# Performance work log

Measured on AMD Instinct MI355X. Metric: run time of the kernel, lower is better.

The kernel has to match this reference:

```python
import jax, jax.numpy as jnp
import numpy as np

EPS = 1e-5
MIN_NORM = 1e-15


def artanh(x):
    return jnp.arctanh(jnp.clip(x, -1.0 + EPS, 1.0 - EPS))


def expmap0(u, c):
    # Poincare ball exponential map at the origin (HGCN style)
    sqrt_c = jnp.sqrt(c)
    u_norm = jnp.maximum(jnp.linalg.norm(u, axis=-1, keepdims=True), MIN_NORM)
    return jnp.tanh(sqrt_c * u_norm) * u / (sqrt_c * u_norm)


def mobius_add(x, y, c):
    x2 = jnp.sum(x * x, axis=-1, keepdims=True)
    y2 = jnp.sum(y * y, axis=-1, keepdims=True)
    xy = jnp.sum(x * y, axis=-1, keepdims=True)
    num = (1.0 + 2.0 * c * xy + c * y2) * x + (1.0 - c * x2) * y
    den = 1.0 + 2.0 * c * xy + (c ** 2) * x2 * y2
    return num / jnp.maximum(den, MIN_NORM)


def sqdist(x, y, c):
    sqrt_c = jnp.sqrt(c)
    ma = mobius_add(-x, y, c)
    dist = (2.0 / sqrt_c) * artanh(sqrt_c * jnp.linalg.norm(ma, axis=-1))
    return dist ** 2


def setup_inputs() -> dict:
    key = jax.random.key(0)
    k1, k2 = jax.random.split(key)
    B, T, N, C, K = 8, 12, 325, 32, 100
    # scale down so points land well inside the unit ball (curvature c=1)
    node_repr = 0.05 * jax.random.normal(k1, (B, T, N, C), dtype=jnp.float32)
    centroid_weight = 0.05 * jax.random.normal(k2, (K, C), dtype=jnp.float32)
    c = jnp.ones((1,), dtype=jnp.float32)
    return {"node_repr": node_repr, "centroid_weight": centroid_weight, "c": c}


def reference(node_repr, centroid_weight, c):
    cc = c[0]
    B, T, N, C = node_repr.shape
    # centroid embedding lookup of arange(K) == the weight table itself
    centroids = expmap0(centroid_weight, cc)          # [K, C]
    x = node_repr[..., None, :]                        # [B, T, N, 1, C]
    node_centroid_dist = sqdist(x, centroids, cc)      # [B, T, N, K] via broadcast
    graph_centroid_dist = jnp.sum(node_centroid_dist, axis=1) / N  # [B, N, K] (faithful to dim=1 in source)
    return graph_centroid_dist, node_centroid_dist
```

## Files before the change

kernel.cpp:

```cpp
#include <hip/hip_runtime.h>

namespace {
constexpr int B = 8, T = 12, N = 325, C = 32, K = 100;
constexpr int NPB = 5;
constexpr int NPAIRS = N / NPB;
constexpr int KT = 7;
constexpr int KP = KT * 16;
constexpr float EPSF = 1e-5f;
constexpr float MIN_NORM = 1e-15f;
}

typedef __attribute__((ext_vector_type(8))) short bf16x8;
typedef __attribute__((ext_vector_type(4))) float f32x4;

__device__ __forceinline__ unsigned short bf16_rne(float x) {
  unsigned int u = __float_as_uint(x);
  unsigned int r = u + 0x7FFFu + ((u >> 16) & 1u);
  return (unsigned short)(r >> 16);
}
__device__ __forceinline__ float bf16_f(unsigned short h) {
  return __uint_as_float(((unsigned int)h) << 16);
}

__global__ __launch_bounds__(320) void hcd_kernel(
    const float* __restrict__ x_g,
    const float* __restrict__ cw,
    const float* __restrict__ cptr,
    float* __restrict__ out0,
    float* __restrict__ out1)
{
  __shared__ unsigned short yh[KP][C];
  __shared__ unsigned short ylo[KP][C];
  __shared__ float y2l[KP];
  __shared__ float x2l[NPB][T];

  const int tid = threadIdx.x;
  const int b  = blockIdx.x / NPAIRS;
  const int np = blockIdx.x % NPAIRS;
  const int n0 = np * NPB;
  const float c  = cptr[0];
  const float sc = sqrtf(c);
  const float inv_c4 = 4.f / c;
  const float HLN2 = 0.34657359028f;
  const float TLOG2E = 2.88539008178f;

  if (tid < KP) {
    float y[C];
    float y2 = 0.f;
    if (tid < K) {
      float u2 = 0.f;
      #pragma unroll
      for (int q = 0; q < C / 4; ++q) {
        float4 v = *(const float4*)(cw + tid * C + 4 * q);
        y[4*q+0] = v.x; y[4*q+1] = v.y; y[4*q+2] = v.z; y[4*q+3] = v.w;
      }
      #pragma unroll
      for (int i = 0; i < C; ++i) u2 = fmaf(y[i], y[i], u2);
      float z = sc * fmaxf(sqrtf(u2), MIN_NORM);
      float E  = exp2f(z * TLOG2E);
      float th = (E - 1.f) * __builtin_amdgcn_rcpf(E + 1.f);
      float f  = th * __builtin_amdgcn_rcpf(z);
      #pragma unroll
      for (int i = 0; i < C; ++i) y[i] *= f;
      y2 = f * f * u2;
    } else {
      #pragma unroll
      for (int i = 0; i < C; ++i) y[i] = 0.f;
    }
    #pragma unroll
    for (int i = 0; i < C; ++i) {
      unsigned short h = bf16_rne(y[i]);
      yh[tid][i]  = h;
      ylo[tid][i] = bf16_rne(y[i] - bf16_f(h));
    }
    y2l[tid] = y2;
  }

  if (tid >= 128 && tid < 128 + NPB * T) {
    int i  = tid - 128;
    int nl = i / T, t = i - nl * T;
    const float* xr = x_g + ((size_t)(b * T + t) * N + (n0 + nl)) * C;
    float s = 0.f;
    #pragma unroll
    for (int q = 0; q < C / 4; ++q) {
      float4 v = *(const float4*)(xr + 4 * q);
      s = fmaf(v.x, v.x, s); s = fmaf(v.y, v.y, s);
      s = fmaf(v.z, v.z, s); s = fmaf(v.w, v.w, s);
    }
    x2l[nl][t] = s;
  }

  const int wave = tid >> 6;
  const int lane = tid & 63;
  const int l16  = lane & 15;
  const int g    = lane >> 4;
  const int n    = n0 + wave;

  const int trow = (l16 < T) ? l16 : 0;
  const float* xrow = x_g + (((size_t)(b * T + trow) * N + n) * C) + 8 * g;
  float4 v0 = *(const float4*)(xrow);
  float4 v1 = *(const float4*)(xrow + 4);
  if (l16 >= T) { v0 = make_float4(0,0,0,0); v1 = make_float4(0,0,0,0); }
  float xe[8] = {v0.x, v0.y, v0.z, v0.w, v1.x, v1.y, v1.z, v1.w};
  bf16x8 ah, al;
  #pragma unroll
  for (int i = 0; i < 8; ++i) {
    unsigned short h = bf16_rne(xe[i]);
    ah[i] = (short)h;
    al[i] = (short)bf16_rne(xe[i] - bf16_f(h));
  }
  __syncthreads();

  bf16x8 bh[KT], bl[KT];
  #pragma unroll
  for (int kt = 0; kt < KT; ++kt) {
    bh[kt] = *(const bf16x8*)&yh [16 * kt + l16][8 * g];
    bl[kt] = *(const bf16x8*)&ylo[16 * kt + l16][8 * g];
  }

  f32x4 acc[KT];
  #pragma unroll
  for (int kt = 0; kt < KT; ++kt) {
    f32x4 a = {0.f, 0.f, 0.f, 0.f};
    a = __builtin_amdgcn_mfma_f32_16x16x32_bf16(al, bh[kt], a, 0, 0, 0);
    a = __builtin_amdgcn_mfma_f32_16x16x32_bf16(ah, bl[kt], a, 0, 0, 0);
    a = __builtin_amdgcn_mfma_f32_16x16x32_bf16(ah, bh[kt], a, 0, 0, 0);
    acc[kt] = a;
  }

  const float c2 = c * c;
  const float tc = 2.f * c;
  float x2r[4];
  #pragma unroll
  for (int reg = 0; reg < 4; ++reg) {
    int t = 4 * g + reg;
    x2r[reg] = x2l[wave][(t < T) ? t : 0];
  }

  #pragma unroll
  for (int kt = 0; kt < KT; ++kt) {
    const int k = 16 * kt + l16;
    const bool kv = (k < K);
    const float y2 = y2l[16 * kt + l16];
    float ps = 0.f;
    #pragma unroll
    for (int reg = 0; reg < 4; ++reg) {
      const int t = 4 * g + reg;
      const bool tv = (t < T);
      const float dot = acc[kt][reg];
      const float x2 = x2r[reg];
      const float xy = -dot;
      const float A  = fmaf(tc, xy, 1.f) + c * y2;
      const float Bc = 1.f - c * x2;
      float num2 = A * A * x2 + Bc * Bc * y2 + 2.f * A * Bc * xy;
      num2 = fmaxf(num2, 0.f);
      float den = fmaf(c2 * x2, y2, fmaf(tc, xy, 1.f));
      den = fmaxf(den, MIN_NORM);
      float s_ = sc * __builtin_amdgcn_sqrtf(num2);
      s_ = fminf(s_, (1.f - EPSF) * den);
      float r  = (den + s_) * __builtin_amdgcn_rcpf(den - s_);
      float at = HLN2 * __builtin_amdgcn_logf(r);
      float d2 = inv_c4 * at * at;
      if (tv & kv)
        out1[(((size_t)(b * T + t)) * N + n) * K + k] = d2;
      ps += tv ? d2 : 0.f;
    }
    ps += __shfl_xor(ps, 16);
    ps += __shfl_xor(ps, 32);
    if (g == 0 && kv)
      out0[((size_t)b * N + n) * K + k] = ps * (1.f / (float)N);
  }
}

extern "C" void kernel_launch(void* const* d_in, const int* in_sizes, int n_in,
                              void* d_out, int out_size, void* d_ws, size_t ws_size,
                              hipStream_t stream) {
  const void* xp = nullptr; const void* cwp = nullptr; const void* cp = nullptr;
  for (int i = 0; i < n_in; ++i) {
    if (in_sizes[i] == B * T * N * C)      xp  = d_in[i];
    else if (in_sizes[i] == K * C)         cwp = d_in[i];
    else if (in_sizes[i] == 1)             cp  = d_in[i];
  }
  if (!xp)  xp  = d_in[0];
  if (!cwp) cwp = d_in[1];
  if (!cp)  cp  = d_in[n_in - 1];

  float* out0 = (float*)d_out;
  float* out1 = out0 + (size_t)B * N * K;

  hipLaunchKernelGGL(hcd_kernel, dim3(B * NPAIRS), dim3(320), 0, stream,
                     (const float*)xp, (const float*)cwp, (const float*)cp,
                     out0, out1);
}
```

Measured before the change: 17.69 us.

## Split centroid dimension across two blocks per node group

Each block now handles only half of the centroids (64 or 36), doubling the grid from 520 to 1040 blocks, and fuses the MFMA with the epilogue per k-tile instead of holding all accumulators. This raises parallelism across the CUs and cuts per-thread register pressure, with launch_bounds now requesting 4 blocks. The cost is duplicated x loading, x-norm computation and bf16 split per block, and an uneven split where the second half has 3 tiles against 4.

Result: slower. 18.12 us (+2.5%).

```diff
diff --git a/kernel.cpp b/kernel.cpp
--- a/kernel.cpp
+++ b/kernel.cpp
@@ -4,8 +4,7 @@
 constexpr int B = 8, T = 12, N = 325, C = 32, K = 100;
 constexpr int NPB = 5;
 constexpr int NPAIRS = N / NPB;
-constexpr int KT = 7;
-constexpr int KP = KT * 16;
+constexpr int KHALF = 64;
 constexpr float EPSF = 1e-5f;
 constexpr float MIN_NORM = 1e-15f;
 }
@@ -22,36 +21,42 @@
   return __uint_as_float(((unsigned int)h) << 16);
 }
 
-__global__ __launch_bounds__(320) void hcd_kernel(
+__global__ __launch_bounds__(320, 4) void hcd_kernel(
     const float* __restrict__ x_g,
     const float* __restrict__ cw,
     const float* __restrict__ cptr,
     float* __restrict__ out0,
     float* __restrict__ out1)
 {
-  __shared__ unsigned short yh[KP][C];
-  __shared__ unsigned short ylo[KP][C];
-  __shared__ float y2l[KP];
+  __shared__ unsigned short yh[KHALF][C];
+  __shared__ unsigned short ylo[KHALF][C];
+  __shared__ float y2l[KHALF];
   __shared__ float x2l[NPB][T];
 
   const int tid = threadIdx.x;
-  const int b  = blockIdx.x / NPAIRS;
-  const int np = blockIdx.x % NPAIRS;
-  const int n0 = np * NPB;
+  const int bx  = blockIdx.x;
+  const int b   = bx / (NPAIRS * 2);
+  const int rem = bx - b * (NPAIRS * 2);
+  const int np  = rem >> 1;
+  const int h   = rem & 1;
+  const int n0  = np * NPB;
+  const int k0  = h * KHALF;
+
   const float c  = cptr[0];
   const float sc = sqrtf(c);
   const float inv_c4 = 4.f / c;
   const float HLN2 = 0.34657359028f;
   const float TLOG2E = 2.88539008178f;
 
-  if (tid < KP) {
+  if (tid < KHALF) {
+    const int kg = k0 + tid;
     float y[C];
     float y2 = 0.f;
-    if (tid < K) {
+    if (kg < K) {
       float u2 = 0.f;
       #pragma unroll
       for (int q = 0; q < C / 4; ++q) {
-        float4 v = *(const float4*)(cw + tid * C + 4 * q);
+        float4 v = *(const float4*)(cw + kg * C + 4 * q);
         y[4*q+0] = v.x; y[4*q+1] = v.y; y[4*q+2] = v.z; y[4*q+3] = v.w;
       }
       #pragma unroll
@@ -69,15 +74,15 @@
     }
     #pragma unroll
     for (int i = 0; i < C; ++i) {
-      unsigned short h = bf16_rne(y[i]);
-      yh[tid][i]  = h;
-      ylo[tid][i] = bf16_rne(y[i] - bf16_f(h));
+      unsigned short hi = bf16_rne(y[i]);
+      yh[tid][i]  = hi;
+      ylo[tid][i] = bf16_rne(y[i] - bf16_f(hi));
     }
     y2l[tid] = y2;
   }
 
-  if (tid >= 128 && tid < 128 + NPB * T) {
-    int i  = tid - 128;
+  if (tid >= 64 && tid < 64 + NPB * T) {
+    int i  = tid - 64;
     int nl = i / T, t = i - nl * T;
     const float* xr = x_g + ((size_t)(b * T + t) * N + (n0 + nl)) * C;
     float s = 0.f;
@@ -90,11 +95,11 @@
     x2l[nl][t] = s;
   }
 
-  const int wave = tid >> 6;
+  const int w    = tid >> 6;
   const int lane = tid & 63;
   const int l16  = lane & 15;
   const int g    = lane >> 4;
-  const int n    = n0 + wave;
+  const int n    = n0 + w;
 
   const int trow = (l16 < T) ? l16 : 0;
   const float* xrow = x_g + (((size_t)(b * T + trow) * N + n) * C) + 8 * g;
@@ -105,70 +110,63 @@
   bf16x8 ah, al;
   #pragma unroll
   for (int i = 0; i < 8; ++i) {
-    unsigned short h = bf16_rne(xe[i]);
-    ah[i] = (short)h;
-    al[i] = (short)bf16_rne(xe[i] - bf16_f(h));
+    unsigned short hi = bf16_rne(xe[i]);
+    ah[i] = (short)hi;
+    al[i] = (short)bf16_rne(xe[i] - bf16_f(hi));
   }
   __syncthreads();
 
-  bf16x8 bh[KT], bl[KT];
-  #pragma unroll
-  for (int kt = 0; kt < KT; ++kt) {
-    bh[kt] = *(const bf16x8*)&yh [16 * kt + l16][8 * g];
-    bl[kt] = *(const bf16x8*)&ylo[16 * kt + l16][8 * g];
-  }
-
-  f32x4 acc[KT];
-  #pragma unroll
-  for (int kt = 0; kt < KT; ++kt) {
-    f32x4 a = {0.f, 0.f, 0.f, 0.f};
-    a = __builtin_amdgcn_mfma_f32_16x16x32_bf16(al, bh[kt], a, 0, 0, 0);
-    a = __builtin_amdgcn_mfma_f32_16x16x32_bf16(ah, bl[kt], a, 0, 0, 0);
-    a = __builtin_amdgcn_mfma_f32_16x16x32_bf16(ah, bh[kt], a, 0, 0, 0);
-    acc[kt] = a;
-  }
-
+  const int nkt = 4 - h;
   const float c2 = c * c;
   const float tc = 2.f * c;
   float x2r[4];
   #pragma unroll
   for (int reg = 0; reg < 4; ++reg) {
     int t = 4 * g + reg;
-    x2r[reg] = x2l[wave][(t < T) ? t : 0];
+    x2r[reg] = x2l[w][(t < T) ? t : 0];
   }
 
   #pragma unroll
-  for (int kt = 0; kt < KT; ++kt) {
-    const int k = 16 * kt + l16;
-    const bool kv = (k < K);
-    const float y2 = y2l[16 * kt + l16];
-    float ps = 0.f;
-    #pragma unroll
-    for (int reg = 0; reg < 4; ++reg) {
-      const int t = 4 * g + reg;
-      const bool tv = (t < T);
-      const float dot = acc[kt][reg];
-      const float x2 = x2r[reg];
-      const float xy = -dot;
-      const float A  = fmaf(tc, xy, 1.f) + c * y2;
-      const float Bc = 1.f - c * x2;
-      float num2 = A * A * x2 + Bc * Bc * y2 + 2.f * A * Bc * xy;
-      num2 = fmaxf(num2, 0.f);
-      float den = fmaf(c2 * x2, y2, fmaf(tc, xy, 1.f));
-      den = fmaxf(den, MIN_NORM);
-      float s_ = sc * __builtin_amdgcn_sqrtf(num2);
-      s_ = fminf(s_, (1.f - EPSF) * den);
-      float r  = (den + s_) * __builtin_amdgcn_rcpf(den - s_);
-      float at = HLN2 * __builtin_amdgcn_logf(r);
-      float d2 = inv_c4 * at * at;
-      if (tv & kv)
-        out1[(((size_t)(b * T + t)) * N + n) * K + k] = d2;
-      ps += tv ? d2 : 0.f;
+  for (int kt = 0; kt < 4; ++kt) {
+    if (kt < nkt) {
+      bf16x8 bhf = *(const bf16x8*)&yh [16 * kt + l16][8 * g];
+      bf16x8 blf = *(const bf16x8*)&ylo[16 * kt + l16][8 * g];
+      f32x4 a = {0.f, 0.f, 0.f, 0.f};
+      a = __builtin_amdgcn_mfma_f32_16x16x32_bf16(al, bhf, a, 0, 0, 0);
+      a = __builtin_amdgcn_mfma_f32_16x16x32_bf16(ah, blf, a, 0, 0, 0);
+      a = __builtin_amdgcn_mfma_f32_16x16x32_bf16(ah, bhf, a, 0, 0, 0);
+
+      const int k = k0 + 16 * kt + l16;
+      const bool kv = (k < K);
+      const float y2 = y2l[16 * kt + l16];
+      float ps = 0.f;
+      #pragma unroll
+      for (int reg = 0; reg < 4; ++reg) {
+        const int t = 4 * g + reg;
+        const bool tv = (t < T);
+        const float dot = a[reg];
+        const float x2 = x2r[reg];
+        const float xy = -dot;
+        const float A  = fmaf(tc, xy, 1.f) + c * y2;
+        const float Bc = 1.f - c * x2;
+        float num2 = A * A * x2 + Bc * Bc * y2 + 2.f * A * Bc * xy;
+        num2 = fmaxf(num2, 0.f);
+        float den = fmaf(c2 * x2, y2, fmaf(tc, xy, 1.f));
+        den = fmaxf(den, MIN_NORM);
+        float s_ = sc * __builtin_amdgcn_sqrtf(num2);
+        s_ = fminf(s_, (1.f - EPSF) * den);
+        float r  = (den + s_) * __builtin_amdgcn_rcpf(den - s_);
+        float at = HLN2 * __builtin_amdgcn_logf(r);
+        float d2 = inv_c4 * at * at;
+        if (tv & kv)
+          out1[(((size_t)(b * T + t)) * N + n) * K + k] = d2;
+        ps += tv ? d2 : 0.f;
+      }
+      ps += __shfl_xor(ps, 16);
+      ps += __shfl_xor(ps, 32);
+      if (g == 0 && kv)
+        out0[((size_t)b * N + n) * K + k] = ps * (1.f / (float)N);
     }
-    ps += __shfl_xor(ps, 16);
-    ps += __shfl_xor(ps, 32);
-    if (g == 0 && kv)
-      out0[((size_t)b * N + n) * K + k] = ps * (1.f / (float)N);
   }
 }
 
@@ -188,7 +186,7 @@
   float* out0 = (float*)d_out;
   float* out1 = out0 + (size_t)B * N * K;
 
-  hipLaunchKernelGGL(hcd_kernel, dim3(B * NPAIRS), dim3(320), 0, stream,
+  hipLaunchKernelGGL(hcd_kernel, dim3(B * NPAIRS * 2), dim3(320), 0, stream,
                      (const float*)xp, (const float*)cwp, (const float*)cp,
                      out0, out1);
 }
```
